# Performance work log

Hardware: AMD Instinct MI355X
Metric: run time of the kernel (lower is better)

The kernel has to match this reference:

```python
import jax, jax.numpy as jnp
import numpy as np

B, N, E, H = 4, 4096, 1024, 16
D = E // H            # head_dim = 64
P_DIM = 64            # proj_dim; feature dim = 2*P_DIM = 128
EPS = 1e-4


def setup_inputs() -> dict:
    key = jax.random.key(0)
    ks = jax.random.split(key, 9)
    x = jax.random.normal(ks[0], (B, N, E), jnp.float32)
    init = 0.02
    Wq = jax.random.normal(ks[1], (E, E), jnp.float32) * init
    Wk = jax.random.normal(ks[2], (E, E), jnp.float32) * init
    Wv = jax.random.normal(ks[3], (E, E), jnp.float32) * init
    Wo = jax.random.normal(ks[4], (E, E), jnp.float32) * init
    bq = jnp.zeros((E,), jnp.float32)
    bk = jnp.zeros((E,), jnp.float32)
    bv = jnp.zeros((E,), jnp.float32)
    bo = jnp.zeros((E,), jnp.float32)
    # orthogonal random projection matrix (proj_dim, head_dim), fixed (non-trainable)
    g = np.random.default_rng(0).normal(size=(P_DIM, D))
    P = jnp.asarray(np.linalg.qr(g)[0], jnp.float32)
    return dict(x=x, Wq=Wq, bq=bq, Wk=Wk, bk=bk, Wv=Wv, bv=bv, Wo=Wo, bo=bo, P=P)


def _heads(z):
    # (B, N, E) -> (B, H, N, D)
    return z.reshape(B, N, H, D).transpose(0, 2, 1, 3)


def _normalize(z):
    return z / (jnp.linalg.norm(z, axis=-1, keepdims=True) + EPS)


def reference(x, Wq, bq, Wk, bk, Wv, bv, Wo, bo, P):
    q = _heads(x @ Wq.T + bq)
    k = _heads(x @ Wk.T + bk)
    v = _heads(x @ Wv.T + bv)
    q = _normalize(q)
    k = _normalize(k)
    scale = H ** 0.25
    qp = jnp.einsum('bhnd,ed->bhne', q, P) * scale
    kp = jnp.einsum('bhnd,ed->bhne', k, P) * scale
    fscale = P_DIM ** (-0.5)   # x.shape[-1]**-0.5 with last dim = proj_dim
    qf = jnp.concatenate([jnp.sin(qp), jnp.cos(qp)], axis=-1) * fscale  # (B,H,N,2p)
    kf = jnp.concatenate([jnp.sin(kp), jnp.cos(kp)], axis=-1) * fscale
    # non-causal linear attention: q @ (k^T v)
    kv = jnp.einsum('bhme,bhmd->bhed', kf, v)          # (B,H,2p,D)
    o = jnp.einsum('bhne,bhed->bhnd', qf, kv)          # (B,H,N,D)
    o = o.transpose(0, 2, 1, 3).reshape(B, N, E)
    return o @ Wo.T + bo
```

## Files before the change

kernel.cpp:

```cpp
#include <hip/hip_runtime.h>
#include <hip/hip_bf16.h>
#include <stdint.h>


typedef __bf16 bf16x8 __attribute__((ext_vector_type(8)));
typedef float f32x4 __attribute__((ext_vector_type(4)));

#define AS1 __attribute__((address_space(1)))
#define AS3 __attribute__((address_space(3)))

__device__ __forceinline__ void gl2lds16(const void* g, void* l) {
    __builtin_amdgcn_global_load_lds((const AS1 void*)g, (AS3 void*)l, 16, 0, 0);
}

static constexpr int GM = 16384, GN = 1024, GK = 1024;
static constexpr int KV_SLABS = 8;

__global__ void detect_kernel(const unsigned short* __restrict__ x,
                              int* __restrict__ flag) {
    __shared__ int s;
    const int lane = threadIdx.x;
    if (lane == 0) s = 0;
    __syncthreads();
    int cnt = 0;
#pragma unroll
    for (int i = 0; i < 2; ++i) {
        const unsigned short u = x[i * 64 + lane];
        const int e = (u >> 7) & 0xFF;
        cnt += (e >= 117 && e <= 131) ? 1 : 0;
    }
    atomicAdd(&s, cnt);
    __syncthreads();
    if (lane == 0) *flag = (s >= 100) ? 1 : 0;
}

__global__ __launch_bounds__(256) void cvt_kernel(
    const void* __restrict__ src, __hip_bfloat16* __restrict__ dst,
    int n, const int* __restrict__ flag) {
    if (*flag) return;
    const int i = (blockIdx.x * 256 + threadIdx.x) * 8;
    if (i >= n) return;
    const float* s = (const float*)src + i;
    const float4 a = *(const float4*)s;
    const float4 b = *(const float4*)(s + 4);
    union { uint4 u; __hip_bfloat16 h[8]; } pk;
    pk.h[0] = __float2bfloat16(a.x); pk.h[1] = __float2bfloat16(a.y);
    pk.h[2] = __float2bfloat16(a.z); pk.h[3] = __float2bfloat16(a.w);
    pk.h[4] = __float2bfloat16(b.x); pk.h[5] = __float2bfloat16(b.y);
    pk.h[6] = __float2bfloat16(b.z); pk.h[7] = __float2bfloat16(b.w);
    *(uint4*)(dst + i) = pk.u;
}

__global__ __launch_bounds__(256, 2) void gemm1m2_kernel(
    const void* __restrict__ Adirect,
    const __hip_bfloat16* __restrict__ Acvt,
    const void* __restrict__ Wr, const __hip_bfloat16* __restrict__ Wc,
    const void* __restrict__ bias_raw,
    void* __restrict__ Cout,
    const int* __restrict__ flag, int last)
{
    __shared__ unsigned short smem[3 * 128 * 64];
    unsigned short* sA0 = smem;
    unsigned short* sA1 = smem + 128 * 64;
    unsigned short* sB  = smem + 2 * 128 * 64;

    const int tid  = threadIdx.x;
    const int lane = tid & 63;
    const int w    = tid >> 6;
    const int wm   = w >> 1, wn = w & 1;
    const int lr   = lane & 15, lk = lane >> 4;

    const int id   = blockIdx.x;
    const int xcd  = id & 7;
    const int s    = id >> 3;
    const int m0   = (xcd * 8 + (s & 7)) * 256;
    const int n0   = (s >> 3) * 128;
    const int fl   = *flag;

    const __hip_bfloat16* A = fl ? (const __hip_bfloat16*)Adirect : Acvt;
    const __hip_bfloat16* W = fl ? (const __hip_bfloat16*)Wr : Wc;

    f32x4 acc[2][4][4];
#pragma unroll
    for (int t = 0; t < 2; ++t)
#pragma unroll
        for (int i = 0; i < 4; ++i)
#pragma unroll
            for (int j = 0; j < 4; ++j)
                acc[t][i][j] = (f32x4){0.f, 0.f, 0.f, 0.f};

    const __hip_bfloat16* Ab0 = A + (size_t)m0 * GK;
    const __hip_bfloat16* Ab1 = A + (size_t)(m0 + 128) * GK;
    const __hip_bfloat16* Wb  = W + (size_t)n0 * GK;

    for (int k0 = 0; k0 < GK; k0 += 64) {
#pragma unroll
        for (int j = 0; j < 4; ++j) {
            const int chunk = j * 256 + tid;
            const int row   = chunk >> 3;
            const int c     = chunk & 7;
            const int cs    = c ^ (row & 7);
            const size_t go = (size_t)row * GK + k0 + cs * 8;
            const int lo = (j * 256 + w * 64) * 16;
            gl2lds16(Ab0 + go, (char*)sA0 + lo);
            gl2lds16(Ab1 + go, (char*)sA1 + lo);
            gl2lds16(Wb  + go, (char*)sB  + lo);
        }
        __syncthreads();
#pragma unroll
        for (int kk = 0; kk < 64; kk += 32) {
            const int jj = ((kk >> 3) + lk) ^ (lr & 7);
            bf16x8 a0f[4], a1f[4], bfr[4];
#pragma unroll
            for (int i = 0; i < 4; ++i)
                a0f[i] = *(const bf16x8*)&sA0[(wm * 64 + i * 16 + lr) * 64 + jj * 8];
#pragma unroll
            for (int i = 0; i < 4; ++i)
                a1f[i] = *(const bf16x8*)&sA1[(wm * 64 + i * 16 + lr) * 64 + jj * 8];
#pragma unroll
            for (int j = 0; j < 4; ++j)
                bfr[j] = *(const bf16x8*)&sB[(wn * 64 + j * 16 + lr) * 64 + jj * 8];
#pragma unroll
            for (int i = 0; i < 4; ++i)
#pragma unroll
                for (int j = 0; j < 4; ++j) {
                    acc[0][i][j] = __builtin_amdgcn_mfma_f32_16x16x32_bf16(
                        a0f[i], bfr[j], acc[0][i][j], 0, 0, 0);
                    acc[1][i][j] = __builtin_amdgcn_mfma_f32_16x16x32_bf16(
                        a1f[i], bfr[j], acc[1][i][j], 0, 0, 0);
                }
        }
        __syncthreads();
    }

    const bool f32out = (last != 0) && (fl == 0);
    if (f32out) {
#pragma unroll
        for (int t = 0; t < 2; ++t)
#pragma unroll
            for (int j = 0; j < 4; ++j) {
                const int col = n0 + wn * 64 + j * 16 + lr;
                const float bv = ((const float*)bias_raw)[col];
#pragma unroll
                for (int i = 0; i < 4; ++i) {
                    const int rbase = m0 + t * 128 + wm * 64 + i * 16 + lk * 4;
#pragma unroll
                    for (int r = 0; r < 4; ++r)
                        ((float*)Cout)[(size_t)(rbase + r) * GN + col] = acc[t][i][j][r] + bv;
                }
            }
        return;
    }
    __hip_bfloat16* sC = (__hip_bfloat16*)smem;
#pragma unroll
    for (int t = 0; t < 2; ++t) {
#pragma unroll
        for (int j = 0; j < 4; ++j) {
            const int col = wn * 64 + j * 16 + lr;
            const float bv = fl ? __bfloat162float(((const __hip_bfloat16*)bias_raw)[n0 + col])
                                : ((const float*)bias_raw)[n0 + col];
            const int c2 = col >> 3, o = col & 7;
#pragma unroll
            for (int i = 0; i < 4; ++i) {
                const int rb = wm * 64 + i * 16 + lk * 4;
#pragma unroll
                for (int r = 0; r < 4; ++r) {
                    const int row = rb + r;
                    sC[row * 128 + (c2 ^ (row & 7)) * 8 + o] =
                        __float2bfloat16(acc[t][i][j][r] + bv);
                }
            }
        }
        __syncthreads();
        {
            const int row = tid >> 1, hf = tid & 1;
            __hip_bfloat16* dst = (__hip_bfloat16*)Cout +
                (size_t)(m0 + t * 128 + row) * GN + n0 + hf * 64;
#pragma unroll
            for (int q = 0; q < 8; ++q) {
                const int cc = (hf * 8 + q) ^ (row & 7);
                *(uint4*)(dst + q * 8) = *(const uint4*)&sC[row * 128 + cc * 8];
            }
        }
        __syncthreads();
    }
}

__global__ __launch_bounds__(256, 2) void gemm2_kernel(
    const void* __restrict__ Adirect,
    const __hip_bfloat16* __restrict__ Acvt,
    const void* __restrict__ W0r, const __hip_bfloat16* __restrict__ W0c,
    const void* __restrict__ W1r, const __hip_bfloat16* __restrict__ W1c,
    const void* __restrict__ b0r, const void* __restrict__ b1r,
    void* __restrict__ o0, void* __restrict__ o1,
    const int* __restrict__ flag)
{
    __shared__ unsigned short smem[3 * 128 * 64];
    unsigned short* sA  = smem;
    unsigned short* sB0 = smem + 128 * 64;
    unsigned short* sB1 = smem + 2 * 128 * 64;

    const int tid  = threadIdx.x;
    const int lane = tid & 63;
    const int w    = tid >> 6;
    const int wm   = w >> 1, wn = w & 1;
    const int lr   = lane & 15, lk = lane >> 4;

    const int id    = blockIdx.x;
    const int xcd   = id & 7;
    const int slot  = id >> 3;
    const int m0    = (xcd * 16 + (slot & 15)) * 128;
    const int n0    = (slot >> 4) * 128;
    const int fl    = *flag;

    const __hip_bfloat16* A  = fl ? (const __hip_bfloat16*)Adirect : Acvt;
    const __hip_bfloat16* W0 = fl ? (const __hip_bfloat16*)W0r : W0c;
    const __hip_bfloat16* W1 = fl ? (const __hip_bfloat16*)W1r : W1c;

    f32x4 acc[2][4][4];
#pragma unroll
    for (int t = 0; t < 2; ++t)
#pragma unroll
        for (int i = 0; i < 4; ++i)
#pragma unroll
            for (int j = 0; j < 4; ++j)
                acc[t][i][j] = (f32x4){0.f, 0.f, 0.f, 0.f};

    const __hip_bfloat16* Ab  = A + (size_t)m0 * GK;
    const __hip_bfloat16* W0b = W0 + (size_t)n0 * GK;
    const __hip_bfloat16* W1b = W1 + (size_t)n0 * GK;

    for (int k0 = 0; k0 < GK; k0 += 64) {
#pragma unroll
        for (int j = 0; j < 4; ++j) {
            const int chunk = j * 256 + tid;
            const int row   = chunk >> 3;
            const int c     = chunk & 7;
            const int cs    = c ^ (row & 7);
            const size_t go = (size_t)row * GK + k0 + cs * 8;
            const int lo = (j * 256 + w * 64) * 16;
            gl2lds16(Ab  + go, (char*)sA  + lo);
            gl2lds16(W0b + go, (char*)sB0 + lo);
            gl2lds16(W1b + go, (char*)sB1 + lo);
        }
        __syncthreads();
#pragma unroll
        for (int kk = 0; kk < 64; kk += 32) {
            const int jj = ((kk >> 3) + lk) ^ (lr & 7);
            bf16x8 af[4], b0f[4], b1f[4];
#pragma unroll
            for (int i = 0; i < 4; ++i)
                af[i] = *(const bf16x8*)&sA[(wm * 64 + i * 16 + lr) * 64 + jj * 8];
#pragma unroll
            for (int j = 0; j < 4; ++j)
                b0f[j] = *(const bf16x8*)&sB0[(wn * 64 + j * 16 + lr) * 64 + jj * 8];
#pragma unroll
            for (int j = 0; j < 4; ++j)
                b1f[j] = *(const bf16x8*)&sB1[(wn * 64 + j * 16 + lr) * 64 + jj * 8];
#pragma unroll
            for (int i = 0; i < 4; ++i)
#pragma unroll
                for (int j = 0; j < 4; ++j) {
                    acc[0][i][j] = __builtin_amdgcn_mfma_f32_16x16x32_bf16(
                        af[i], b0f[j], acc[0][i][j], 0, 0, 0);
                    acc[1][i][j] = __builtin_amdgcn_mfma_f32_16x16x32_bf16(
                        af[i], b1f[j], acc[1][i][j], 0, 0, 0);
                }
        }
        __syncthreads();
    }

    __hip_bfloat16* sC = (__hip_bfloat16*)smem;
#pragma unroll
    for (int t = 0; t < 2; ++t) {
        const void* bias_raw = t ? b1r : b0r;
        void* Cout = t ? o1 : o0;
#pragma unroll
        for (int j = 0; j < 4; ++j) {
            const int col = wn * 64 + j * 16 + lr;
            const float bv = fl ? __bfloat162float(((const __hip_bfloat16*)bias_raw)[n0 + col])
                                : ((const float*)bias_raw)[n0 + col];
            const int c2 = col >> 3, o = col & 7;
#pragma unroll
            for (int i = 0; i < 4; ++i) {
                const int rb = wm * 64 + i * 16 + lk * 4;
#pragma unroll
                for (int r = 0; r < 4; ++r) {
                    const int row = rb + r;
                    sC[row * 128 + (c2 ^ (row & 7)) * 8 + o] =
                        __float2bfloat16(acc[t][i][j][r] + bv);
                }
            }
        }
        __syncthreads();
        {
            const int row = tid >> 1, hf = tid & 1;
            __hip_bfloat16* dst = (__hip_bfloat16*)Cout + (size_t)(m0 + row) * GN + n0 + hf * 64;
#pragma unroll
            for (int q = 0; q < 8; ++q) {
                const int cc = (hf * 8 + q) ^ (row & 7);
                *(uint4*)(dst + q * 8) = *(const uint4*)&sC[row * 128 + cc * 8];
            }
        }
        __syncthreads();
    }
}

__device__ __forceinline__ void load_P(const void* Praw, int f,
                                       __hip_bfloat16* sP, int tid) {
    const int e = tid >> 2, q = tid & 3;
    union { uint4 u[2]; __hip_bfloat16 h[16]; } pk;
    if (f) {
        pk.u[0] = *(const uint4*)((const __hip_bfloat16*)Praw + e * 64 + q * 16);
        pk.u[1] = *(const uint4*)((const __hip_bfloat16*)Praw + e * 64 + q * 16 + 8);
    } else {
        const float* ps = (const float*)Praw + e * 64 + q * 16;
#pragma unroll
        for (int j = 0; j < 16; ++j) pk.h[j] = __float2bfloat16(ps[j]);
    }
    *(uint4*)&sP[e * 72 + q * 16]     = pk.u[0];
    *(uint4*)&sP[e * 72 + q * 16 + 8] = pk.u[1];
}

__device__ __forceinline__ float sumsq16(uint4 a, uint4 b) {
    union { uint4 u; __hip_bfloat16 h[8]; } x0, x1;
    x0.u = a; x1.u = b;
    float ss = 0.f;
#pragma unroll
    for (int j = 0; j < 8; ++j) {
        float v0 = __bfloat162float(x0.h[j]); ss += v0 * v0;
        float v1 = __bfloat162float(x1.h[j]); ss += v1 * v1;
    }
    return ss;
}

__global__ __launch_bounds__(256) void kv_kernel(
    const __hip_bfloat16* __restrict__ Km,
    const __hip_bfloat16* __restrict__ Vm,
    const void* __restrict__ Praw,
    float* __restrict__ PKV,
    const int* __restrict__ flag)
{
    __shared__ __hip_bfloat16 sK[64 * 72];
    __shared__ __hip_bfloat16 sVT[64 * 72];
    __shared__ __hip_bfloat16 sP[64 * 72];
    __shared__ __hip_bfloat16 sKFT[128 * 72];
    __shared__ float sRN[64];

    const int tid  = threadIdx.x;
    const int lane = tid & 63;
    const int w    = tid >> 6;
    const int lr   = lane & 15, lk = lane >> 4;
    const int bh   = blockIdx.y;
    const int b    = bh >> 4, h = bh & 15;
    const int nst  = blockIdx.x * 512;
    const int f    = *flag;
    const int n    = tid >> 2, q2 = tid & 3;

    load_P(Praw, f, sP, tid);

    f32x4 acck[2][4];
#pragma unroll
    for (int i = 0; i < 2; ++i)
#pragma unroll
        for (int j = 0; j < 4; ++j)
            acck[i][j] = (f32x4){0.f, 0.f, 0.f, 0.f};

    size_t base = ((size_t)(b * 4096 + nst + n)) * 1024 + h * 64 + q2 * 16;
    uint4 ka = *(const uint4*)(Km + base), kb = *(const uint4*)(Km + base + 8);
    uint4 va = *(const uint4*)(Vm + base), vb = *(const uint4*)(Vm + base + 8);

    for (int s = 0; s < 8; ++s) {
        __syncthreads();
        *(uint4*)&sK[n * 72 + q2 * 16]     = ka;
        *(uint4*)&sK[n * 72 + q2 * 16 + 8] = kb;
        {
            union { uint4 u[2]; __hip_bfloat16 h[16]; } vv;
            vv.u[0] = va; vv.u[1] = vb;
#pragma unroll
            for (int j = 0; j < 16; ++j) sVT[(q2 * 16 + j) * 72 + n] = vv.h[j];
        }
        {
            float ss = sumsq16(ka, kb);
            ss += __shfl_xor(ss, 1, 64);
            ss += __shfl_xor(ss, 2, 64);
            if (q2 == 0) sRN[n] = 2.0f / (sqrtf(ss) + 1e-4f);
        }
        if (s < 7) {
            base = ((size_t)(b * 4096 + nst + (s + 1) * 64 + n)) * 1024 + h * 64 + q2 * 16;
            ka = *(const uint4*)(Km + base); kb = *(const uint4*)(Km + base + 8);
            va = *(const uint4*)(Vm + base); vb = *(const uint4*)(Vm + base + 8);
        }
        {
            bf16x8 afr0 = *(const bf16x8*)&sK[(w * 16 + lr) * 72 + lk * 8];
            bf16x8 afr1 = *(const bf16x8*)&sK[(w * 16 + lr) * 72 + 32 + lk * 8];
            float rn[4];
#pragma unroll
            for (int r = 0; r < 4; ++r) rn[r] = sRN[w * 16 + lk * 4 + r];
#pragma unroll
            for (int eb = 0; eb < 4; ++eb) {
                f32x4 pa = (f32x4){0.f, 0.f, 0.f, 0.f};
                bf16x8 b0 = *(const bf16x8*)&sP[(eb * 16 + lr) * 72 + lk * 8];
                bf16x8 b1 = *(const bf16x8*)&sP[(eb * 16 + lr) * 72 + 32 + lk * 8];
                pa = __builtin_amdgcn_mfma_f32_16x16x32_bf16(afr0, b0, pa, 0, 0, 0);
                pa = __builtin_amdgcn_mfma_f32_16x16x32_bf16(afr1, b1, pa, 0, 0, 0);
                const int col = eb * 16 + lr;
#pragma unroll
                for (int r = 0; r < 4; ++r) {
                    const int row = w * 16 + lk * 4 + r;
                    float sv, cv;
                    __sincosf(pa[r] * rn[r], &sv, &cv);
                    sKFT[col * 72 + row]        = __float2bfloat16(sv * 0.125f);
                    sKFT[(col + 64) * 72 + row] = __float2bfloat16(cv * 0.125f);
                }
            }
        }
        __syncthreads();
#pragma unroll
        for (int ks = 0; ks < 2; ++ks) {
            bf16x8 a2[2], b2[4];
            a2[0] = *(const bf16x8*)&sKFT[(w * 16 + lr) * 72 + ks * 32 + lk * 8];
            a2[1] = *(const bf16x8*)&sKFT[((w + 4) * 16 + lr) * 72 + ks * 32 + lk * 8];
#pragma unroll
            for (int db = 0; db < 4; ++db)
                b2[db] = *(const bf16x8*)&sVT[(db * 16 + lr) * 72 + ks * 32 + lk * 8];
#pragma unroll
            for (int i = 0; i < 2; ++i)
#pragma unroll
                for (int db = 0; db < 4; ++db)
                    acck[i][db] = __builtin_amdgcn_mfma_f32_16x16x32_bf16(
                        a2[i], b2[db], acck[i][db], 0, 0, 0);
        }
    }

    float* out = PKV + ((size_t)blockIdx.x * 64 + bh) * 8192;
#pragma unroll
    for (int i = 0; i < 2; ++i)
#pragma unroll
        for (int db = 0; db < 4; ++db)
#pragma unroll
            for (int r = 0; r < 4; ++r) {
                const int e = (w + 4 * i) * 16 + lk * 4 + r;
                const int d = db * 16 + lr;
                out[e * 64 + d] = acck[i][db][r];
            }
}

__global__ __launch_bounds__(256) void kv_reduce_kernel(
    const float* __restrict__ PKV, float* __restrict__ gKV)
{
    const int i = (blockIdx.x * 256 + threadIdx.x) * 4;
    f32x4 s = (f32x4){0.f, 0.f, 0.f, 0.f};
#pragma unroll
    for (int sl = 0; sl < KV_SLABS; ++sl) {
        const float4 v = *(const float4*)(PKV + (size_t)sl * 64 * 8192 + i);
        s[0] += v.x; s[1] += v.y; s[2] += v.z; s[3] += v.w;
    }
    *(float4*)(gKV + i) = *(float4*)&s;
}

__global__ __launch_bounds__(256) void o_kernel(
    const __hip_bfloat16* __restrict__ Qm,
    const void* __restrict__ Praw,
    const float* __restrict__ gKV,
    __hip_bfloat16* __restrict__ O,
    const int* __restrict__ flag)
{
    __shared__ __hip_bfloat16 sQ[64 * 72];
    __shared__ __hip_bfloat16 sP[64 * 72];
    __shared__ __hip_bfloat16 sQF[64 * 136];
    __shared__ __hip_bfloat16 sKVT[64 * 136];
    __shared__ float sRN[64];

    const int tid  = threadIdx.x;
    const int lane = tid & 63;
    const int w    = tid >> 6;
    const int lr   = lane & 15, lk = lane >> 4;
    const int bh   = blockIdx.y;
    const int b    = bh >> 4, h = bh & 15;
    const int nst  = blockIdx.x * 256;
    const int f    = *flag;
    const int n    = tid >> 2, q2 = tid & 3;

    load_P(Praw, f, sP, tid);
    {
        const float* kvsrc = gKV + (size_t)bh * 8192;
        for (int t = tid; t < 8192; t += 256) {
            const int e = t >> 6, d = t & 63;
            sKVT[d * 136 + e] = __float2bfloat16(kvsrc[t]);
        }
    }

    size_t base = ((size_t)(b * 4096 + nst + n)) * 1024 + h * 64 + q2 * 16;
    uint4 qa = *(const uint4*)(Qm + base), qb = *(const uint4*)(Qm + base + 8);

    __syncthreads();

    for (int s = 0; s < 4; ++s) {
        const int gn0 = nst + s * 64;
        *(uint4*)&sQ[n * 72 + q2 * 16]     = qa;
        *(uint4*)&sQ[n * 72 + q2 * 16 + 8] = qb;
        {
            float ss = sumsq16(qa, qb);
            ss += __shfl_xor(ss, 1, 64);
            ss += __shfl_xor(ss, 2, 64);
            if (q2 == 0) sRN[n] = 2.0f / (sqrtf(ss) + 1e-4f);
        }
        if (s < 3) {
            base = ((size_t)(b * 4096 + nst + (s + 1) * 64 + n)) * 1024 + h * 64 + q2 * 16;
            qa = *(const uint4*)(Qm + base); qb = *(const uint4*)(Qm + base + 8);
        }
        {
            bf16x8 afr0 = *(const bf16x8*)&sQ[(w * 16 + lr) * 72 + lk * 8];
            bf16x8 afr1 = *(const bf16x8*)&sQ[(w * 16 + lr) * 72 + 32 + lk * 8];
            float rn[4];
#pragma unroll
            for (int r = 0; r < 4; ++r) rn[r] = sRN[w * 16 + lk * 4 + r];
#pragma unroll
            for (int eb = 0; eb < 4; ++eb) {
                f32x4 pa = (f32x4){0.f, 0.f, 0.f, 0.f};
                bf16x8 b0 = *(const bf16x8*)&sP[(eb * 16 + lr) * 72 + lk * 8];
                bf16x8 b1 = *(const bf16x8*)&sP[(eb * 16 + lr) * 72 + 32 + lk * 8];
                pa = __builtin_amdgcn_mfma_f32_16x16x32_bf16(afr0, b0, pa, 0, 0, 0);
                pa = __builtin_amdgcn_mfma_f32_16x16x32_bf16(afr1, b1, pa, 0, 0, 0);
                const int col = eb * 16 + lr;
#pragma unroll
                for (int r = 0; r < 4; ++r) {
                    const int row = w * 16 + lk * 4 + r;
                    float sv, cv;
                    __sincosf(pa[r] * rn[r], &sv, &cv);
                    sQF[row * 136 + col]      = __float2bfloat16(sv * 0.125f);
                    sQF[row * 136 + 64 + col] = __float2bfloat16(cv * 0.125f);
                }
            }
        }
        f32x4 oacc[4];
#pragma unroll
        for (int nb = 0; nb < 4; ++nb) oacc[nb] = (f32x4){0.f, 0.f, 0.f, 0.f};
#pragma unroll
        for (int ks = 0; ks < 4; ++ks) {
            bf16x8 aa = *(const bf16x8*)&sQF[(w * 16 + lr) * 136 + ks * 32 + lk * 8];
#pragma unroll
            for (int nb = 0; nb < 4; ++nb) {
                bf16x8 bb = *(const bf16x8*)&sKVT[(nb * 16 + lr) * 136 + ks * 32 + lk * 8];
                oacc[nb] = __builtin_amdgcn_mfma_f32_16x16x32_bf16(aa, bb, oacc[nb], 0, 0, 0);
            }
        }
#pragma unroll
        for (int nb = 0; nb < 4; ++nb)
#pragma unroll
            for (int r = 0; r < 4; ++r)
                sQ[(w * 16 + lk * 4 + r) * 72 + nb * 16 + lr] =
                    __float2bfloat16(oacc[nb][r]);
        {
            uint4 o0 = *(uint4*)&sQ[n * 72 + q2 * 16];
            uint4 o1 = *(uint4*)&sQ[n * 72 + q2 * 16 + 8];
            const size_t obase = ((size_t)(b * 4096 + gn0 + n)) * 1024 + h * 64 + q2 * 16;
            *(uint4*)(O + obase)     = o0;
            *(uint4*)(O + obase + 8) = o1;
        }
    }
}

extern "C" void kernel_launch(void* const* d_in, const int* in_sizes, int n_in,
                              void* d_out, int out_size, void* d_ws, size_t ws_size,
                              hipStream_t stream)
{
    (void)in_sizes; (void)n_in; (void)out_size; (void)ws_size;
    const void* x  = d_in[0];
    const void* Wq = d_in[1];
    const void* bq = d_in[2];
    const void* Wk = d_in[3];
    const void* bk = d_in[4];
    const void* Wv = d_in[5];
    const void* bv = d_in[6];
    const void* Wo = d_in[7];
    const void* bo = d_in[8];
    const void* P  = d_in[9];

    constexpr size_t XE = (size_t)GM * GN;
    constexpr size_t WE = (size_t)GN * GK;
    constexpr size_t KVE = (size_t)64 * 128 * 64;

    __hip_bfloat16* xb  = (__hip_bfloat16*)d_ws;
    __hip_bfloat16* wqb = xb + XE;
    __hip_bfloat16* wkb = wqb + WE;
    __hip_bfloat16* wvb = wkb + WE;
    __hip_bfloat16* wob = wvb + WE;
    __hip_bfloat16* R1  = wob + WE;
    __hip_bfloat16* R2  = R1 + XE;
    float* gKV = (float*)(R2 + XE);
    float* PKV = gKV + KVE;
    int* flag  = (int*)(PKV + (size_t)KV_SLABS * 64 * 8192);

    dim3 blk(256);
    hipLaunchKernelGGL(detect_kernel, dim3(1), dim3(64), 0, stream,
                       (const unsigned short*)x, flag);

    hipLaunchKernelGGL(cvt_kernel, dim3(8192), blk, 0, stream, x,  xb,  (int)XE, flag);
    hipLaunchKernelGGL(cvt_kernel, dim3(512),  blk, 0, stream, Wq, wqb, (int)WE, flag);
    hipLaunchKernelGGL(cvt_kernel, dim3(512),  blk, 0, stream, Wk, wkb, (int)WE, flag);
    hipLaunchKernelGGL(cvt_kernel, dim3(512),  blk, 0, stream, Wv, wvb, (int)WE, flag);
    hipLaunchKernelGGL(cvt_kernel, dim3(512),  blk, 0, stream, Wo, wob, (int)WE, flag);

    hipLaunchKernelGGL(gemm2_kernel, dim3(1024), blk, 0, stream,
                       x, xb, Wk, wkb, Wv, wvb, bk, bv, R1, R2, flag);
    hipLaunchKernelGGL(kv_kernel, dim3(KV_SLABS, 64), blk, 0, stream, R1, R2, P, PKV, flag);
    hipLaunchKernelGGL(kv_reduce_kernel, dim3(512), blk, 0, stream, PKV, gKV);
    hipLaunchKernelGGL(gemm1m2_kernel, dim3(512), blk, 0, stream,
                       x, xb, Wq, wqb, bq, R2, flag, 0);
    hipLaunchKernelGGL(o_kernel, dim3(16, 64), blk, 0, stream, R2, P, gKV, R1, flag);
    hipLaunchKernelGGL(gemm1m2_kernel, dim3(512), blk, 0, stream,
                       R1, R1, Wo, wob, bo, d_out, flag, 1);
}
```

Before: 362.5 us.

## Replace GEMMs with 256x256 double-buffered 512-thread kernel, split fused K/V GEMM

```diff
diff --git a/kernel.cpp b/kernel.cpp
--- a/kernel.cpp
+++ b/kernel.cpp
@@ -51,7 +51,7 @@
     *(uint4*)(dst + i) = pk.u;
 }
 
-__global__ __launch_bounds__(256, 2) void gemm1m2_kernel(
+__global__ __launch_bounds__(512, 1) void gemm256_kernel(
     const void* __restrict__ Adirect,
     const __hip_bfloat16* __restrict__ Acvt,
     const void* __restrict__ Wr, const __hip_bfloat16* __restrict__ Wc,
@@ -59,250 +59,139 @@
     void* __restrict__ Cout,
     const int* __restrict__ flag, int last)
 {
-    __shared__ unsigned short smem[3 * 128 * 64];
-    unsigned short* sA0 = smem;
-    unsigned short* sA1 = smem + 128 * 64;
-    unsigned short* sB  = smem + 2 * 128 * 64;
+    __shared__ unsigned short smem[65536];
 
     const int tid  = threadIdx.x;
     const int lane = tid & 63;
     const int w    = tid >> 6;
-    const int wm   = w >> 1, wn = w & 1;
+    const int wm   = w >> 2, wn = w & 3;
     const int lr   = lane & 15, lk = lane >> 4;
 
-    const int id   = blockIdx.x;
-    const int xcd  = id & 7;
-    const int s    = id >> 3;
-    const int m0   = (xcd * 8 + (s & 7)) * 256;
-    const int n0   = (s >> 3) * 128;
-    const int fl   = *flag;
+    const int id  = blockIdx.x;
+    const int xcd = id & 7;
+    const int s   = id >> 3;
+    const int m0  = (xcd * 8 + (s >> 2)) * 256;
+    const int n0  = (s & 3) * 256;
+    const int fl  = *flag;
 
     const __hip_bfloat16* A = fl ? (const __hip_bfloat16*)Adirect : Acvt;
     const __hip_bfloat16* W = fl ? (const __hip_bfloat16*)Wr : Wc;
-
-    f32x4 acc[2][4][4];
-#pragma unroll
-    for (int t = 0; t < 2; ++t)
-#pragma unroll
-        for (int i = 0; i < 4; ++i)
-#pragma unroll
-            for (int j = 0; j < 4; ++j)
-                acc[t][i][j] = (f32x4){0.f, 0.f, 0.f, 0.f};
-
-    const __hip_bfloat16* Ab0 = A + (size_t)m0 * GK;
-    const __hip_bfloat16* Ab1 = A + (size_t)(m0 + 128) * GK;
-    const __hip_bfloat16* Wb  = W + (size_t)n0 * GK;
-
-    for (int k0 = 0; k0 < GK; k0 += 64) {
+    const __hip_bfloat16* Ab = A + (size_t)m0 * GK;
+    const __hip_bfloat16* Wb = W + (size_t)n0 * GK;
+
+    f32x4 acc[8][4];
+#pragma unroll
+    for (int i = 0; i < 8; ++i)
+#pragma unroll
+        for (int j = 0; j < 4; ++j)
+            acc[i][j] = (f32x4){0.f, 0.f, 0.f, 0.f};
+
+    auto stage = [&](int p, int k0) {
+        unsigned short* dA = smem + p * 32768;
+        unsigned short* dB = dA + 16384;
 #pragma unroll
         for (int j = 0; j < 4; ++j) {
-            const int chunk = j * 256 + tid;
+            const int chunk = j * 512 + tid;
             const int row   = chunk >> 3;
             const int c     = chunk & 7;
             const int cs    = c ^ (row & 7);
             const size_t go = (size_t)row * GK + k0 + cs * 8;
-            const int lo = (j * 256 + w * 64) * 16;
-            gl2lds16(Ab0 + go, (char*)sA0 + lo);
-            gl2lds16(Ab1 + go, (char*)sA1 + lo);
-            gl2lds16(Wb  + go, (char*)sB  + lo);
-        }
-        __syncthreads();
-#pragma unroll
-        for (int kk = 0; kk < 64; kk += 32) {
-            const int jj = ((kk >> 3) + lk) ^ (lr & 7);
-            bf16x8 a0f[4], a1f[4], bfr[4];
-#pragma unroll
-            for (int i = 0; i < 4; ++i)
-                a0f[i] = *(const bf16x8*)&sA0[(wm * 64 + i * 16 + lr) * 64 + jj * 8];
-#pragma unroll
-            for (int i = 0; i < 4; ++i)
-                a1f[i] = *(const bf16x8*)&sA1[(wm * 64 + i * 16 + lr) * 64 + jj * 8];
+            const int lo = (j * 512 + w * 64) * 16;
+            gl2lds16(Ab + go, (char*)dA + lo);
+            gl2lds16(Wb + go, (char*)dB + lo);
+        }
+    };
+
+    auto compute = [&](int p) {
+        const unsigned short* cA = smem + p * 32768;
+        const unsigned short* cB = cA + 16384;
+#pragma unroll
+        for (int ks = 0; ks < 2; ++ks) {
+            const int jj = (ks * 4 + lk) ^ (lr & 7);
+            bf16x8 bfr[4];
 #pragma unroll
             for (int j = 0; j < 4; ++j)
-                bfr[j] = *(const bf16x8*)&sB[(wn * 64 + j * 16 + lr) * 64 + jj * 8];
-#pragma unroll
-            for (int i = 0; i < 4; ++i)
-#pragma unroll
-                for (int j = 0; j < 4; ++j) {
-                    acc[0][i][j] = __builtin_amdgcn_mfma_f32_16x16x32_bf16(
-                        a0f[i], bfr[j], acc[0][i][j], 0, 0, 0);
-                    acc[1][i][j] = __builtin_amdgcn_mfma_f32_16x16x32_bf16(
-                        a1f[i], bfr[j], acc[1][i][j], 0, 0, 0);
-                }
-        }
-        __syncthreads();
-    }
+                bfr[j] = *(const bf16x8*)&cB[(wn * 64 + j * 16 + lr) * 64 + jj * 8];
+            __builtin_amdgcn_s_setprio(1);
+#pragma unroll
+            for (int i = 0; i < 8; ++i) {
+                const bf16x8 af =
+                    *(const bf16x8*)&cA[(wm * 128 + i * 16 + lr) * 64 + jj * 8];
+#pragma unroll
+                for (int j = 0; j < 4; ++j)
+                    acc[i][j] = __builtin_amdgcn_mfma_f32_16x16x32_bf16(
+                        af, bfr[j], acc[i][j], 0, 0, 0);
+            }
+            __builtin_amdgcn_s_setprio(0);
+        }
+    };
+
+    constexpr int NT = GK / 64;
+    stage(0, 0);
+    int p = 0;
+    for (int kt = 0; kt < NT - 1; ++kt) {
+        stage(p ^ 1, (kt + 1) * 64);
+        asm volatile("s_waitcnt vmcnt(8)" ::: "memory");
+        __builtin_amdgcn_s_barrier();
+        compute(p);
+        asm volatile("s_waitcnt lgkmcnt(0)" ::: "memory");
+        __builtin_amdgcn_s_barrier();
+        p ^= 1;
+    }
+    asm volatile("s_waitcnt vmcnt(0)" ::: "memory");
+    __builtin_amdgcn_s_barrier();
+    compute(p);
+    asm volatile("s_waitcnt lgkmcnt(0)" ::: "memory");
+    __builtin_amdgcn_s_barrier();
 
     const bool f32out = (last != 0) && (fl == 0);
     if (f32out) {
 #pragma unroll
-        for (int t = 0; t < 2; ++t)
-#pragma unroll
-            for (int j = 0; j < 4; ++j) {
-                const int col = n0 + wn * 64 + j * 16 + lr;
-                const float bv = ((const float*)bias_raw)[col];
-#pragma unroll
-                for (int i = 0; i < 4; ++i) {
-                    const int rbase = m0 + t * 128 + wm * 64 + i * 16 + lk * 4;
-#pragma unroll
-                    for (int r = 0; r < 4; ++r)
-                        ((float*)Cout)[(size_t)(rbase + r) * GN + col] = acc[t][i][j][r] + bv;
-                }
-            }
+        for (int j = 0; j < 4; ++j) {
+            const int col = n0 + wn * 64 + j * 16 + lr;
+            const float bv = ((const float*)bias_raw)[col];
+#pragma unroll
+            for (int i = 0; i < 8; ++i) {
+                const int rbase = m0 + wm * 128 + i * 16 + lk * 4;
+#pragma unroll
+                for (int r = 0; r < 4; ++r)
+                    ((float*)Cout)[(size_t)(rbase + r) * GN + col] =
+                        acc[i][j][r] + bv;
+            }
+        }
         return;
     }
-    __hip_bfloat16* sC = (__hip_bfloat16*)smem;
-#pragma unroll
-    for (int t = 0; t < 2; ++t) {
-#pragma unroll
-        for (int j = 0; j < 4; ++j) {
-            const int col = wn * 64 + j * 16 + lr;
-            const float bv = fl ? __bfloat162float(((const __hip_bfloat16*)bias_raw)[n0 + col])
-                                : ((const float*)bias_raw)[n0 + col];
-            const int c2 = col >> 3, o = col & 7;
-#pragma unroll
-            for (int i = 0; i < 4; ++i) {
-                const int rb = wm * 64 + i * 16 + lk * 4;
-#pragma unroll
-                for (int r = 0; r < 4; ++r) {
-                    const int row = rb + r;
-                    sC[row * 128 + (c2 ^ (row & 7)) * 8 + o] =
-                        __float2bfloat16(acc[t][i][j][r] + bv);
-                }
-            }
-        }
-        __syncthreads();
-        {
-            const int row = tid >> 1, hf = tid & 1;
-            __hip_bfloat16* dst = (__hip_bfloat16*)Cout +
-                (size_t)(m0 + t * 128 + row) * GN + n0 + hf * 64;
-#pragma unroll
-            for (int q = 0; q < 8; ++q) {
-                const int cc = (hf * 8 + q) ^ (row & 7);
-                *(uint4*)(dst + q * 8) = *(const uint4*)&sC[row * 128 + cc * 8];
-            }
-        }
-        __syncthreads();
-    }
-}
-
-__global__ __launch_bounds__(256, 2) void gemm2_kernel(
-    const void* __restrict__ Adirect,
-    const __hip_bfloat16* __restrict__ Acvt,
-    const void* __restrict__ W0r, const __hip_bfloat16* __restrict__ W0c,
-    const void* __restrict__ W1r, const __hip_bfloat16* __restrict__ W1c,
-    const void* __restrict__ b0r, const void* __restrict__ b1r,
-    void* __restrict__ o0, void* __restrict__ o1,
-    const int* __restrict__ flag)
-{
-    __shared__ unsigned short smem[3 * 128 * 64];
-    unsigned short* sA  = smem;
-    unsigned short* sB0 = smem + 128 * 64;
-    unsigned short* sB1 = smem + 2 * 128 * 64;
-
-    const int tid  = threadIdx.x;
-    const int lane = tid & 63;
-    const int w    = tid >> 6;
-    const int wm   = w >> 1, wn = w & 1;
-    const int lr   = lane & 15, lk = lane >> 4;
-
-    const int id    = blockIdx.x;
-    const int xcd   = id & 7;
-    const int slot  = id >> 3;
-    const int m0    = (xcd * 16 + (slot & 15)) * 128;
-    const int n0    = (slot >> 4) * 128;
-    const int fl    = *flag;
-
-    const __hip_bfloat16* A  = fl ? (const __hip_bfloat16*)Adirect : Acvt;
-    const __hip_bfloat16* W0 = fl ? (const __hip_bfloat16*)W0r : W0c;
-    const __hip_bfloat16* W1 = fl ? (const __hip_bfloat16*)W1r : W1c;
-
-    f32x4 acc[2][4][4];
-#pragma unroll
-    for (int t = 0; t < 2; ++t)
-#pragma unroll
-        for (int i = 0; i < 4; ++i)
-#pragma unroll
-            for (int j = 0; j < 4; ++j)
-                acc[t][i][j] = (f32x4){0.f, 0.f, 0.f, 0.f};
-
-    const __hip_bfloat16* Ab  = A + (size_t)m0 * GK;
-    const __hip_bfloat16* W0b = W0 + (size_t)n0 * GK;
-    const __hip_bfloat16* W1b = W1 + (size_t)n0 * GK;
-
-    for (int k0 = 0; k0 < GK; k0 += 64) {
-#pragma unroll
-        for (int j = 0; j < 4; ++j) {
-            const int chunk = j * 256 + tid;
-            const int row   = chunk >> 3;
-            const int c     = chunk & 7;
-            const int cs    = c ^ (row & 7);
-            const size_t go = (size_t)row * GK + k0 + cs * 8;
-            const int lo = (j * 256 + w * 64) * 16;
-            gl2lds16(Ab  + go, (char*)sA  + lo);
-            gl2lds16(W0b + go, (char*)sB0 + lo);
-            gl2lds16(W1b + go, (char*)sB1 + lo);
-        }
-        __syncthreads();
-#pragma unroll
-        for (int kk = 0; kk < 64; kk += 32) {
-            const int jj = ((kk >> 3) + lk) ^ (lr & 7);
-            bf16x8 af[4], b0f[4], b1f[4];
-#pragma unroll
-            for (int i = 0; i < 4; ++i)
-                af[i] = *(const bf16x8*)&sA[(wm * 64 + i * 16 + lr) * 64 + jj * 8];
-#pragma unroll
-            for (int j = 0; j < 4; ++j)
-                b0f[j] = *(const bf16x8*)&sB0[(wn * 64 + j * 16 + lr) * 64 + jj * 8];
-#pragma unroll
-            for (int j = 0; j < 4; ++j)
-                b1f[j] = *(const bf16x8*)&sB1[(wn * 64 + j * 16 + lr) * 64 + jj * 8];
-#pragma unroll
-            for (int i = 0; i < 4; ++i)
-#pragma unroll
-                for (int j = 0; j < 4; ++j) {
-                    acc[0][i][j] = __builtin_amdgcn_mfma_f32_16x16x32_bf16(
-                        af[i], b0f[j], acc[0][i][j], 0, 0, 0);
-                    acc[1][i][j] = __builtin_amdgcn_mfma_f32_16x16x32_bf16(
-                        af[i], b1f[j], acc[1][i][j], 0, 0, 0);
-                }
-        }
-        __syncthreads();
-    }
-
-    __hip_bfloat16* sC = (__hip_bfloat16*)smem;
-#pragma unroll
-    for (int t = 0; t < 2; ++t) {
-        const void* bias_raw = t ? b1r : b0r;
-        void* Cout = t ? o1 : o0;
-#pragma unroll
-        for (int j = 0; j < 4; ++j) {
-            const int col = wn * 64 + j * 16 + lr;
-            const float bv = fl ? __bfloat162float(((const __hip_bfloat16*)bias_raw)[n0 + col])
-                                : ((const float*)bias_raw)[n0 + col];
-            const int c2 = col >> 3, o = col & 7;
-#pragma unroll
-            for (int i = 0; i < 4; ++i) {
-                const int rb = wm * 64 + i * 16 + lk * 4;
-#pragma unroll
-                for (int r = 0; r < 4; ++r) {
-                    const int row = rb + r;
-                    sC[row * 128 + (c2 ^ (row & 7)) * 8 + o] =
-                        __float2bfloat16(acc[t][i][j][r] + bv);
-                }
-            }
-        }
-        __syncthreads();
-        {
-            const int row = tid >> 1, hf = tid & 1;
-            __hip_bfloat16* dst = (__hip_bfloat16*)Cout + (size_t)(m0 + row) * GN + n0 + hf * 64;
-#pragma unroll
-            for (int q = 0; q < 8; ++q) {
-                const int cc = (hf * 8 + q) ^ (row & 7);
-                *(uint4*)(dst + q * 8) = *(const uint4*)&sC[row * 128 + cc * 8];
-            }
-        }
-        __syncthreads();
+
+    unsigned short* sC = smem;
+#pragma unroll
+    for (int j = 0; j < 4; ++j) {
+        const int col = wn * 64 + j * 16 + lr;
+        const float bv = fl ? __bfloat162float(((const __hip_bfloat16*)bias_raw)[n0 + col])
+                            : ((const float*)bias_raw)[n0 + col];
+        const int c_hi = col >> 3, off = col & 7;
+#pragma unroll
+        for (int i = 0; i < 8; ++i) {
+            const int rb = wm * 128 + i * 16 + lk * 4;
+#pragma unroll
+            for (int r = 0; r < 4; ++r) {
+                const int row = rb + r;
+                const int phys = c_hi ^ (row & 7);
+                __hip_bfloat16 hv = __float2bfloat16(acc[i][j][r] + bv);
+                sC[row * 256 + phys * 8 + off] = *(unsigned short*)&hv;
+            }
+        }
+    }
+    __syncthreads();
+    {
+        const int row = tid >> 1, half = tid & 1;
+        __hip_bfloat16* dst = (__hip_bfloat16*)Cout +
+            (size_t)(m0 + row) * GN + n0 + half * 128;
+#pragma unroll
+        for (int q = 0; q < 16; ++q) {
+            const int chunk = half * 16 + q;
+            const int phys  = chunk ^ (row & 7);
+            *(uint4*)(dst + q * 8) = *(const uint4*)&sC[row * 256 + phys * 8];
+        }
     }
 }
 
@@ -603,13 +492,15 @@
     hipLaunchKernelGGL(cvt_kernel, dim3(512),  blk, 0, stream, Wv, wvb, (int)WE, flag);
     hipLaunchKernelGGL(cvt_kernel, dim3(512),  blk, 0, stream, Wo, wob, (int)WE, flag);
 
-    hipLaunchKernelGGL(gemm2_kernel, dim3(1024), blk, 0, stream,
-                       x, xb, Wk, wkb, Wv, wvb, bk, bv, R1, R2, flag);
+    hipLaunchKernelGGL(gemm256_kernel, dim3(256), dim3(512), 0, stream,
+                       x, xb, Wk, wkb, bk, R1, flag, 0);
+    hipLaunchKernelGGL(gemm256_kernel, dim3(256), dim3(512), 0, stream,
+                       x, xb, Wv, wvb, bv, R2, flag, 0);
     hipLaunchKernelGGL(kv_kernel, dim3(KV_SLABS, 64), blk, 0, stream, R1, R2, P, PKV, flag);
     hipLaunchKernelGGL(kv_reduce_kernel, dim3(512), blk, 0, stream, PKV, gKV);
-    hipLaunchKernelGGL(gemm1m2_kernel, dim3(512), blk, 0, stream,
+    hipLaunchKernelGGL(gemm256_kernel, dim3(256), dim3(512), 0, stream,
                        x, xb, Wq, wqb, bq, R2, flag, 0);
     hipLaunchKernelGGL(o_kernel, dim3(16, 64), blk, 0, stream, R2, P, gKV, R1, flag);
-    hipLaunchKernelGGL(gemm1m2_kernel, dim3(512), blk, 0, stream,
+    hipLaunchKernelGGL(gemm256_kernel, dim3(256), dim3(512), 0, stream,
                        R1, R1, Wo, wob, bo, d_out, flag, 1);
 }
```

After: 372.6 us. 2.8% more time.
